# Kernel tuning notes

Measured on AMD Instinct MI355X. Metric: run time of the kernel, lower is better.

The kernel has to match this reference:

```python
import jax, jax.numpy as jnp
import numpy as np

B, S, H, K = 64, 512, 768, 21  # batch, seq_len, bert hidden, num_labels


def setup_inputs() -> dict:
    key = jax.random.key(0)
    ks = jax.random.split(key, 8)
    hidden = jax.random.normal(ks[0], (B, S, H), jnp.float32)  # post-BERT states
    W = jax.random.normal(ks[1], (H, K), jnp.float32) * 0.02    # classifier weight
    b = jnp.zeros((K,), jnp.float32)                            # classifier bias
    start_transitions = jax.random.uniform(ks[2], (K,), jnp.float32, -0.1, 0.1)
    transitions = jax.random.uniform(ks[3], (K, K), jnp.float32, -0.1, 0.1)
    end_transitions = jax.random.uniform(ks[4], (K,), jnp.float32, -0.1, 0.1)
    labels = jax.random.randint(ks[5], (B, S), 0, K)
    # torchcrf requires mask[:, 0] == 1; use variable-length prefix masks
    lengths = jax.random.randint(ks[6], (B,), S // 2, S + 1)
    attention_mask = jnp.arange(S)[None, :] < lengths[:, None]  # [B,S] bool
    return dict(hidden=hidden, W=W, b=b,
                start_transitions=start_transitions,
                transitions=transitions,
                end_transitions=end_transitions,
                labels=labels, attention_mask=attention_mask)


def _crf_nll(logits, labels, mask, start_t, trans, end_t):
    """torchcrf CRF forward (reduction='sum' log-likelihood), negated."""
    fmask = mask.astype(logits.dtype)  # [B,S]
    # ---- numerator: score of the gold path ----
    emit = jnp.take_along_axis(logits, labels[..., None], axis=2)[..., 0]  # [B,S]
    tr = trans[labels[:, :-1], labels[:, 1:]]                              # [B,S-1]
    num = start_t[labels[:, 0]] + emit[:, 0] \
        + jnp.sum((emit[:, 1:] + tr) * fmask[:, 1:], axis=1)
    lengths = mask.sum(axis=1)
    last_tags = jnp.take_along_axis(labels, (lengths - 1)[:, None], axis=1)[:, 0]
    num = num + end_t[last_tags]
    # ---- denominator: forward algorithm (logsumexp recurrence) ----
    alpha0 = start_t[None, :] + logits[:, 0]           # [B,K]
    ems = jnp.swapaxes(logits[:, 1:], 0, 1)            # [S-1,B,K]
    ms = jnp.swapaxes(mask[:, 1:], 0, 1)               # [S-1,B]

    def step(alpha, xs):
        em, m = xs
        nxt = jax.scipy.special.logsumexp(
            alpha[:, :, None] + trans[None, :, :] + em[:, None, :], axis=1)
        return jnp.where(m[:, None], nxt, alpha), None

    alpha, _ = jax.lax.scan(step, alpha0, (ems, ms))
    logZ = jax.scipy.special.logsumexp(alpha + end_t[None, :], axis=1)  # [B]
    return jnp.sum(logZ - num)  # negative log-likelihood (sum over batch)


def reference(hidden, W, b, start_transitions, transitions, end_transitions,
              labels, attention_mask):
    # dropout is identity in eval; the GRU in __init__ is unused in forward
    logits = hidden @ W + b  # [B,S,K]
    nll = _crf_nll(logits, labels, attention_mask,
                   start_transitions, transitions, end_transitions)
    # module returns (logits, -1 * log_likelihood) = (logits, nll)
    return (logits, nll)
```

## Files before the change

### kernel.cpp

```cpp
#include <hip/hip_runtime.h>

#define BSZ 64
#define SEQ 512
#define HID 768
#define NK  21

#define REP21(X) X(0) X(1) X(2) X(3) X(4) X(5) X(6) X(7) X(8) X(9) X(10) \
                 X(11) X(12) X(13) X(14) X(15) X(16) X(17) X(18) X(19) X(20)

__global__ __launch_bounds__(256) void gemm_bias_kernel(
    const float* __restrict__ hidden, const float* __restrict__ W,
    const float* __restrict__ bias, float* __restrict__ out)
{
    __shared__ float hs[2][64 * 65];
    __shared__ float part[4][64 * NK];

    const int tid  = threadIdx.x;
    const int lane = tid & 63;
    const int wv   = __builtin_amdgcn_readfirstlane(tid >> 6);
    const int cw   = tid & 31;
    const int rr   = tid >> 5;

    const float* gbase = hidden + (size_t)blockIdx.x * 64 * HID;

#define DECL(i) float a##i = 0.f;
    REP21(DECL)
#undef DECL

    float st[16];
    #pragma unroll
    for (int sub = 0; sub < 2; ++sub)
        #pragma unroll
        for (int p = 0; p < 8; ++p)
            st[sub * 8 + p] = gbase[(size_t)(p * 8 + rr) * HID + sub * 32 + cw];

    for (int ch = 0; ch < 12; ++ch) {
        float* hb = hs[ch & 1];
        #pragma unroll
        for (int sub = 0; sub < 2; ++sub)
            #pragma unroll
            for (int p = 0; p < 8; ++p)
                hb[(sub * 32 + cw) * 65 + p * 8 + rr] = st[sub * 8 + p];
        __syncthreads();

        if (ch < 11) {
            const float* gsrc = gbase + (ch + 1) * 64;
            #pragma unroll
            for (int sub = 0; sub < 2; ++sub)
                #pragma unroll
                for (int p = 0; p < 8; ++p)
                    st[sub * 8 + p] = gsrc[(size_t)(p * 8 + rr) * HID + sub * 32 + cw];
        }

        const float* wb   = W + (size_t)(ch * 64 + wv * 16) * NK;
        const float* hcol = hb + (size_t)(wv * 16) * 65 + lane;
        #pragma unroll 4
        for (int cc = 0; cc < 16; ++cc) {
            const float h = hcol[cc * 65];
            const float* w = wb + cc * NK;
#define STEP(i) a##i = fmaf(h, w[i], a##i);
            REP21(STEP)
#undef STEP
        }
    }

    float* pp = &part[wv][lane * NK];
#define ST(i) pp[i] = a##i;
    REP21(ST)
#undef ST
    __syncthreads();

    const int base_out = blockIdx.x * (64 * NK);
    for (int idx = tid; idx < 64 * NK; idx += 256) {
        const int k = idx - (idx / NK) * NK;
        const float s = part[0][idx] + part[1][idx] + part[2][idx] + part[3][idx];
        out[base_out + idx] = s + bias[k];
    }
}

__global__ __launch_bounds__(128) void crf_kernel(
    const float* __restrict__ logits,
    const float* __restrict__ start_t,
    const float* __restrict__ trans,
    const float* __restrict__ end_t,
    const int* __restrict__ labels,
    const int* __restrict__ mask,
    float* __restrict__ per_batch)
{
    __shared__ __align__(16) float Xl[SEQ * NK];
    __shared__ float C[SEQ];
    __shared__ float comb[24];

    const int b    = blockIdx.x;
    const int tid  = threadIdx.x;
    const int lane = tid & 63;
    const int wid  = tid >> 6;

    {
        const float4* g4 = (const float4*)(logits + (size_t)b * SEQ * NK);
        float4* l4 = (float4*)Xl;
        for (int idx = tid; idx < SEQ * NK / 4; idx += 128) l4[idx] = g4[idx];
    }

    const int* lab = labels + b * SEQ;
    const int* msk = mask   + b * SEQ;

    int cnt = 0;
    for (int t = lane; t < SEQ; t += 64) cnt += (msk[t] != 0);
    #pragma unroll
    for (int off = 32; off > 0; off >>= 1) cnt += __shfl_xor(cnt, off, 64);
    const int L = cnt;
    const int m = L >> 1;

    __syncthreads();

    {
        float numacc = 0.f;
        for (int t = tid; t < L; t += 128) {
            if (t == 0) numacc += start_t[lab[0]] + Xl[lab[0]];
            else        numacc += Xl[t * NK + lab[t]] + trans[lab[t - 1] * NK + lab[t]];
        }
        if (tid == 0) numacc += end_t[lab[L - 1]];
        #pragma unroll
        for (int off = 32; off > 0; off >>= 1) numacc += __shfl_xor(numacc, off, 64);
        if (lane == 0) comb[22 + wid] = numacc;
    }

    for (int t = tid; t < SEQ; t += 128) C[t] = Xl[t * NK];
    __syncthreads();

    for (int idx = tid; idx < SEQ * NK; idx += 128) {
        const int t = idx / NK;
        Xl[idx] = __expf(Xl[idx] - C[t]);
    }
    __syncthreads();

    const int jj = (lane < NK) ? lane : NK - 1;

#define RL(v, k) __uint_as_float(__builtin_amdgcn_readlane(__float_as_uint(v), k))
#define MATVEC(vv, EE, outv) do {                                          \
    float s0 = RL(vv, 0) * EE[0];                                          \
    float s1 = RL(vv, 1) * EE[1];                                          \
    float s2 = RL(vv, 2) * EE[2];                                          \
    s0 = fmaf(RL(vv,  3), EE[ 3], s0); s1 = fmaf(RL(vv,  4), EE[ 4], s1);  \
    s2 = fmaf(RL(vv,  5), EE[ 5], s2); s0 = fmaf(RL(vv,  6), EE[ 6], s0);  \
    s1 = fmaf(RL(vv,  7), EE[ 7], s1); s2 = fmaf(RL(vv,  8), EE[ 8], s2);  \
    s0 = fmaf(RL(vv,  9), EE[ 9], s0); s1 = fmaf(RL(vv, 10), EE[10], s1);  \
    s2 = fmaf(RL(vv, 11), EE[11], s2); s0 = fmaf(RL(vv, 12), EE[12], s0);  \
    s1 = fmaf(RL(vv, 13), EE[13], s1); s2 = fmaf(RL(vv, 14), EE[14], s2);  \
    s0 = fmaf(RL(vv, 15), EE[15], s0); s1 = fmaf(RL(vv, 16), EE[16], s1);  \
    s2 = fmaf(RL(vv, 17), EE[17], s2); s0 = fmaf(RL(vv, 18), EE[18], s0);  \
    s1 = fmaf(RL(vv, 19), EE[19], s1); s2 = fmaf(RL(vv, 20), EE[20], s2);  \
    outv = (s0 + s1) + s2;                                                 \
} while (0)
#define RENORM() do {                                                      \
    const float mm = __uint_as_float(                                      \
        __builtin_amdgcn_readfirstlane(__float_as_uint(a)));               \
    a *= __builtin_amdgcn_rcpf(mm);                                        \
    Orenorm += __logf(mm);                                                 \
} while (0)

    float a;
    float Orenorm = 0.f;
    float csum = 0.f;

    if (wid == 0) {
        float Ecol[NK];
        #pragma unroll
        for (int k = 0; k < NK; ++k) Ecol[k] = __expf(trans[k * NK + jj]);

        a = __expf(start_t[jj]) * Xl[jj];
        for (int t = lane; t <= m; t += 64) csum += C[t];

#define FSTEP(xr) do { float nv; MATVEC(a, Ecol, nv); a = nv * (xr); } while (0)
        int t0 = 1;
        for (; t0 + 7 <= m; t0 += 8) {
            const float* xb = Xl + t0 * NK + jj;
            const float x0 = xb[0];      const float x1 = xb[NK];
            const float x2 = xb[2 * NK]; const float x3 = xb[3 * NK];
            const float x4 = xb[4 * NK]; const float x5 = xb[5 * NK];
            const float x6 = xb[6 * NK]; const float x7 = xb[7 * NK];
            FSTEP(x0); FSTEP(x1); FSTEP(x2); FSTEP(x3);
            FSTEP(x4); FSTEP(x5); FSTEP(x6); FSTEP(x7);
            RENORM();
        }
        for (; t0 <= m; ++t0) { const float x = Xl[t0 * NK + jj]; FSTEP(x); }
#undef FSTEP
    } else {
        float Erow[NK];
        #pragma unroll
        for (int k = 0; k < NK; ++k) Erow[k] = __expf(trans[jj * NK + k]);

        a = __expf(end_t[jj]);
        for (int t = m + 1 + lane; t < L; t += 64) csum += C[t];

#define BSTEP(xr) do { const float u = a * (xr); float nv; MATVEC(u, Erow, nv); a = nv; } while (0)
        int t0 = L - 1;
        for (; t0 - 7 >= m + 1; t0 -= 8) {
            const float* xb = Xl + t0 * NK + jj;
            const float x0 = xb[0];       const float x1 = xb[-NK];
            const float x2 = xb[-2 * NK]; const float x3 = xb[-3 * NK];
            const float x4 = xb[-4 * NK]; const float x5 = xb[-5 * NK];
            const float x6 = xb[-6 * NK]; const float x7 = xb[-7 * NK];
            BSTEP(x0); BSTEP(x1); BSTEP(x2); BSTEP(x3);
            BSTEP(x4); BSTEP(x5); BSTEP(x6); BSTEP(x7);
            RENORM();
        }
        for (; t0 >= m + 1; --t0) { const float x = Xl[t0 * NK + jj]; BSTEP(x); }
#undef BSTEP
    }
#undef RL
#undef MATVEC
#undef RENORM

    #pragma unroll
    for (int off = 32; off > 0; off >>= 1) csum += __shfl_xor(csum, off, 64);

    if (wid == 1) {
        if (lane < NK) comb[lane] = a;
        if (lane == 0) comb[21] = csum + Orenorm;
    }
    __syncthreads();

    if (wid == 0) {
        float val = (lane < NK) ? a * comb[lane] : 0.f;
        #pragma unroll
        for (int off = 32; off > 0; off >>= 1) val += __shfl_xor(val, off, 64);
        if (lane == 0) {
            const float OF  = csum + Orenorm;
            const float num = comb[22] + comb[23];
            per_batch[b] = OF + comb[21] + __logf(val) - num;
        }
    }
}

__global__ __launch_bounds__(64) void reduce_kernel(
    const float* __restrict__ pb, float* __restrict__ out)
{
    float v = pb[threadIdx.x];
    #pragma unroll
    for (int off = 32; off > 0; off >>= 1) v += __shfl_xor(v, off, 64);
    if (threadIdx.x == 0) out[BSZ * SEQ * NK] = v;
}

extern "C" void kernel_launch(void* const* d_in, const int* in_sizes, int n_in,
                              void* d_out, int out_size, void* d_ws, size_t ws_size,
                              hipStream_t stream)
{
    const float* hidden  = (const float*)d_in[0];
    const float* W       = (const float*)d_in[1];
    const float* bias    = (const float*)d_in[2];
    const float* start_t = (const float*)d_in[3];
    const float* trans   = (const float*)d_in[4];
    const float* end_t   = (const float*)d_in[5];
    const int*   labels  = (const int*)d_in[6];
    const int*   mask    = (const int*)d_in[7];
    float* out = (float*)d_out;
    float* pb  = (float*)d_ws;

    gemm_bias_kernel<<<(BSZ * SEQ) / 64, 256, 0, stream>>>(hidden, W, bias, out);
    crf_kernel<<<BSZ, 128, 0, stream>>>(out, start_t, trans, end_t, labels, mask, pb);
    reduce_kernel<<<1, 64, 0, stream>>>(pb, out);
}
```

Measured before the change: 234.4 us.

## Replace scalar FP32 classifier GEMM with bf16 MFMA 16x16x32

The hidden@W projection used per-thread scalar FMAs over a shared-memory-transposed tile, followed by a cross-wave partial-sum reduction. It now converts each block's hidden rows and a transposed copy of W to bf16 and computes the product with MFMA 16x16x32 instructions. Each wave handles 16 rows and covers the 21 labels with two 16-wide output tiles, so the shared-memory transpose and the reduction buffer go away. In exchange, every block re-converts all of W into shared memory, and the logits lose precision from the bf16 rounding, which also feeds into the CRF loss.

```diff
diff --git a/kernel.cpp b/kernel.cpp
--- a/kernel.cpp
+++ b/kernel.cpp
@@ -5,76 +5,80 @@
 #define HID 768
 #define NK  21
 
-#define REP21(X) X(0) X(1) X(2) X(3) X(4) X(5) X(6) X(7) X(8) X(9) X(10) \
-                 X(11) X(12) X(13) X(14) X(15) X(16) X(17) X(18) X(19) X(20)
-
+typedef short bf16x8 __attribute__((ext_vector_type(8)));
+typedef float f32x4  __attribute__((ext_vector_type(4)));
+
+__device__ __forceinline__ unsigned f2bf_pk(float lo, float hi) {
+    unsigned ul = __float_as_uint(lo);
+    unsigned uh = __float_as_uint(hi);
+    ul = (ul + 0x7fffu + ((ul >> 16) & 1u)) >> 16;
+    uh = (uh + 0x7fffu + ((uh >> 16) & 1u)) >> 16;
+    return ul | (uh << 16);
+}
+
+#define WSTRIDE 784
 __global__ __launch_bounds__(256) void gemm_bias_kernel(
     const float* __restrict__ hidden, const float* __restrict__ W,
     const float* __restrict__ bias, float* __restrict__ out)
 {
-    __shared__ float hs[2][64 * 65];
-    __shared__ float part[4][64 * NK];
+    __shared__ unsigned short WlT[32 * WSTRIDE];
 
     const int tid  = threadIdx.x;
     const int lane = tid & 63;
-    const int wv   = __builtin_amdgcn_readfirstlane(tid >> 6);
-    const int cw   = tid & 31;
-    const int rr   = tid >> 5;
-
-    const float* gbase = hidden + (size_t)blockIdx.x * 64 * HID;
-
-#define DECL(i) float a##i = 0.f;
-    REP21(DECL)
-#undef DECL
-
-    float st[16];
-    #pragma unroll
-    for (int sub = 0; sub < 2; ++sub)
-        #pragma unroll
-        for (int p = 0; p < 8; ++p)
-            st[sub * 8 + p] = gbase[(size_t)(p * 8 + rr) * HID + sub * 32 + cw];
-
-    for (int ch = 0; ch < 12; ++ch) {
-        float* hb = hs[ch & 1];
-        #pragma unroll
-        for (int sub = 0; sub < 2; ++sub)
-            #pragma unroll
-            for (int p = 0; p < 8; ++p)
-                hb[(sub * 32 + cw) * 65 + p * 8 + rr] = st[sub * 8 + p];
-        __syncthreads();
-
-        if (ch < 11) {
-            const float* gsrc = gbase + (ch + 1) * 64;
-            #pragma unroll
-            for (int sub = 0; sub < 2; ++sub)
-                #pragma unroll
-                for (int p = 0; p < 8; ++p)
-                    st[sub * 8 + p] = gsrc[(size_t)(p * 8 + rr) * HID + sub * 32 + cw];
-        }
-
-        const float* wb   = W + (size_t)(ch * 64 + wv * 16) * NK;
-        const float* hcol = hb + (size_t)(wv * 16) * 65 + lane;
-        #pragma unroll 4
-        for (int cc = 0; cc < 16; ++cc) {
-            const float h = hcol[cc * 65];
-            const float* w = wb + cc * NK;
-#define STEP(i) a##i = fmaf(h, w[i], a##i);
-            REP21(STEP)
-#undef STEP
-        }
-    }
-
-    float* pp = &part[wv][lane * NK];
-#define ST(i) pp[i] = a##i;
-    REP21(ST)
-#undef ST
-    __syncthreads();
-
-    const int base_out = blockIdx.x * (64 * NK);
-    for (int idx = tid; idx < 64 * NK; idx += 256) {
-        const int k = idx - (idx / NK) * NK;
-        const float s = part[0][idx] + part[1][idx] + part[2][idx] + part[3][idx];
-        out[base_out + idx] = s + bias[k];
+    const int wv   = tid >> 6;
+    const int n    = lane & 15;
+    const int quad = lane >> 4;
+
+    const int arow = blockIdx.x * 64 + wv * 16 + n;
+    const float* ap = hidden + (size_t)arow * HID + quad * 8;
+
+    float4 c0a = *(const float4*)(ap + 0);
+    float4 c0b = *(const float4*)(ap + 4);
+
+    for (int idx = tid; idx < HID * NK; idx += 256) {
+        const int k = idx / NK;
+        const int nn = idx - k * NK;
+        const unsigned u = __float_as_uint(W[idx]);
+        WlT[nn * WSTRIDE + k] =
+            (unsigned short)((u + 0x7fffu + ((u >> 16) & 1u)) >> 16);
+    }
+    __syncthreads();
+
+    const unsigned short* bp0 = WlT + n * WSTRIDE + quad * 8;
+    const unsigned short* bp1 = WlT + (16 + n) * WSTRIDE + quad * 8;
+
+    f32x4 acc0 = {0.f, 0.f, 0.f, 0.f};
+    f32x4 acc1 = {0.f, 0.f, 0.f, 0.f};
+
+    #pragma unroll
+    for (int c = 0; c < HID / 32; ++c) {
+        float4 c1a, c1b;
+        if (c + 1 < HID / 32) {
+            c1a = *(const float4*)(ap + (c + 1) * 32);
+            c1b = *(const float4*)(ap + (c + 1) * 32 + 4);
+        }
+        union { bf16x8 v; unsigned u[4]; } af;
+        af.u[0] = f2bf_pk(c0a.x, c0a.y);
+        af.u[1] = f2bf_pk(c0a.z, c0a.w);
+        af.u[2] = f2bf_pk(c0b.x, c0b.y);
+        af.u[3] = f2bf_pk(c0b.z, c0b.w);
+
+        const bf16x8 b0 = *(const bf16x8*)(bp0 + c * 32);
+        const bf16x8 b1 = *(const bf16x8*)(bp1 + c * 32);
+
+        acc0 = __builtin_amdgcn_mfma_f32_16x16x32_bf16(af.v, b0, acc0, 0, 0, 0);
+        acc1 = __builtin_amdgcn_mfma_f32_16x16x32_bf16(af.v, b1, acc1, 0, 0, 0);
+        c0a = c1a; c0b = c1b;
+    }
+
+    const float b0v = bias[n];
+    const float b1v = (n < NK - 16) ? bias[16 + n] : 0.f;
+    const int rbase = blockIdx.x * 64 + wv * 16 + quad * 4;
+    #pragma unroll
+    for (int r = 0; r < 4; ++r) {
+        float* op = out + (size_t)(rbase + r) * NK;
+        op[n] = acc0[r] + b0v;
+        if (n < NK - 16) op[16 + n] = acc1[r] + b1v;
     }
 }
 
```

After: 209.0 us. 10.8% less time.
